# Performance work log

Hardware: AMD Instinct MI355X
Metric: run time of the kernel (lower is better)

## Reference

```python
import jax, jax.numpy as jnp
import numpy as np

MUL = 32            # multiplicity of 0e and 1o irreps
IN_DIM = MUL * 4    # 32 scalars + 32 vectors = 128
SH_DIM = 4          # 1x0e + 1x1o
N_EDGE_FEAT = 128
HIDDEN = 128
W_NUMEL = 4 * MUL * MUL  # 4 CG paths, uvw weights 32x1x32 each
EPS = 1e-5
INV_SQRT3 = 1.0 / np.sqrt(3.0)
PATH_NORM = 1.0 / np.sqrt(2.0 * MUL)  # 2 paths per output irrep, fan-in MUL


def _fc(edge_attr, W1, b1, W2, b2):
    h = jax.nn.relu(edge_attr @ W1 + b1)
    return h @ W2 + b2  # [E, W_NUMEL]


def _tensor_product(x, sh, w):
    # FullyConnectedTensorProduct for (32x0e+32x1o) x (1x0e+1x1o) -> (32x0e+32x1o)
    # CG (real w3j): 0x0->0: 1 ; 0x1->1, 1x0->1, 1x1->0: delta/sqrt(3)
    E = x.shape[0]
    x0 = x[:, :MUL]                      # [E,32]   scalars
    x1 = x[:, MUL:].reshape(E, MUL, 3)   # [E,32,3] vectors
    sh0 = sh[:, 0]                       # [E]
    sh1 = sh[:, 1:4]                     # [E,3]
    wA = w[:, 0 * MUL * MUL:1 * MUL * MUL].reshape(E, MUL, MUL)  # 0e x 0e -> 0e
    wB = w[:, 1 * MUL * MUL:2 * MUL * MUL].reshape(E, MUL, MUL)  # 0e x 1o -> 1o
    wC = w[:, 2 * MUL * MUL:3 * MUL * MUL].reshape(E, MUL, MUL)  # 1o x 0e -> 1o
    wD = w[:, 3 * MUL * MUL:4 * MUL * MUL].reshape(E, MUL, MUL)  # 1o x 1o -> 0e
    out0 = PATH_NORM * (
        jnp.einsum('eu,euw->ew', x0 * sh0[:, None], wA)
        + INV_SQRT3 * jnp.einsum('eui,ei,euw->ew', x1, sh1, wD))
    out1 = PATH_NORM * INV_SQRT3 * (
        jnp.einsum('eu,ei,euw->ewi', x0, sh1, wB)
        + jnp.einsum('eui,euw->ewi', x1 * sh0[:, None, None], wC))
    return jnp.concatenate([out0, out1.reshape(E, MUL * 3)], axis=-1)  # [E,128]


def _batch_norm(x, bn_weight, bn_bias):
    # e3nn-style equivariant BatchNorm (training stats): scalars get mean/var
    # normalization + affine; vectors get norm normalization + scale.
    N = x.shape[0]
    s = x[:, :MUL]                       # [N,32]
    v = x[:, MUL:].reshape(N, MUL, 3)    # [N,32,3]
    s = s - s.mean(axis=0)
    s = s * (jax.lax.rsqrt((s ** 2).mean(axis=0) + EPS) * bn_weight[:MUL]) + bn_bias
    v_norm = jax.lax.rsqrt((v ** 2).mean(axis=-1).mean(axis=0) + EPS)  # [32]
    v = v * (v_norm * bn_weight[MUL:])[None, :, None]
    return jnp.concatenate([s, v.reshape(N, MUL * 3)], axis=-1)


def _forward(node_attr, edge_index, edge_attr, edge_sh,
             W1, b1, W2, b2, bn_weight, bn_bias):
    edge_src, edge_dst = edge_index[0], edge_index[1]
    N = node_attr.shape[0]
    w = _fc(edge_attr, W1, b1, W2, b2)                     # [E, 4096]
    tp = _tensor_product(node_attr[edge_dst], edge_sh, w)  # [E, 128]
    # scatter mean over edge_src
    summed = jax.ops.segment_sum(tp, edge_src, num_segments=N)
    counts = jax.ops.segment_sum(jnp.ones((tp.shape[0],), tp.dtype), edge_src,
                                 num_segments=N)
    out = summed / jnp.maximum(counts, 1.0)[:, None]
    out = out + node_attr                                  # residual (same dim, pad=0)
    return _batch_norm(out, bn_weight, bn_bias)


def setup_inputs() -> dict:
    key = jax.random.key(0)
    ks = jax.random.split(key, 10)
    N, E = 10000, 60000
    node_attr = jax.random.normal(ks[0], (N, IN_DIM), jnp.float32)
    edge_index = jax.random.randint(ks[1], (2, E), 0, N)
    edge_attr = jax.random.normal(ks[2], (E, N_EDGE_FEAT), jnp.float32)
    edge_sh = jax.random.normal(ks[3], (E, SH_DIM), jnp.float32)
    W1 = jax.random.normal(ks[4], (N_EDGE_FEAT, HIDDEN), jnp.float32) / np.sqrt(N_EDGE_FEAT)
    b1 = jnp.zeros((HIDDEN,), jnp.float32)
    W2 = jax.random.normal(ks[5], (HIDDEN, W_NUMEL), jnp.float32) / np.sqrt(HIDDEN)
    b2 = jnp.zeros((W_NUMEL,), jnp.float32)
    bn_weight = jnp.ones((2 * MUL,), jnp.float32)
    bn_bias = jnp.zeros((MUL,), jnp.float32)
    return {"node_attr": node_attr, "edge_index": edge_index,
            "edge_attr": edge_attr, "edge_sh": edge_sh,
            "W1": W1, "b1": b1, "W2": W2, "b2": b2,
            "bn_weight": bn_weight, "bn_bias": bn_bias}


def reference(node_attr, edge_index, edge_attr, edge_sh,
              W1, b1, W2, b2, bn_weight, bn_bias):
    return _forward(node_attr, edge_index, edge_attr, edge_sh,
                    W1, b1, W2, b2, bn_weight, bn_bias)
```

## Files before the change

### kernel.cpp

```cpp
#include <hip/hip_runtime.h>
#include <math.h>

#define EPSV 1e-5f
#define IS3  0.57735026918962576f
#define PNRM 0.125f

typedef __attribute__((ext_vector_type(8)))  short  short8;
typedef __attribute__((ext_vector_type(16))) float  floatx16;

static __device__ inline unsigned short f2bf(float f) {
    unsigned int u = __float_as_uint(f);
    return (unsigned short)((u + 0x7fff + ((u >> 16) & 1)) >> 16);
}
static __device__ inline float bflo(unsigned int u) { return __uint_as_float(u << 16); }
static __device__ inline float bfhi(unsigned int u) { return __uint_as_float(u & 0xffff0000u); }

#define GLD16(gp, lp) __builtin_amdgcn_global_load_lds( \
    (const __attribute__((address_space(1))) unsigned int*)(gp), \
    (__attribute__((address_space(3))) unsigned int*)(lp), 16, 0, 0)

__global__ __launch_bounds__(256) void k0_sw(const float* __restrict__ src,
                                             unsigned short* __restrict__ dst,
                                             int total, int nc) {
    int i = blockIdx.x * 256 + threadIdx.x;
    if (i >= total) return;
    int tile = i >> 12, t = i & 4095;
    int k = ((t >> 8) << 3) | (t & 7);
    int c = (tile << 5) | ((t >> 3) & 31);
    dst[i] = f2bf(src[(size_t)k * nc + c]);
}

__global__ __launch_bounds__(256) void k1_fc(const float* __restrict__ ea,
                                             const unsigned short* __restrict__ W1T,
                                             const float* __restrict__ b1,
                                             const int* __restrict__ ei,
                                             unsigned short* __restrict__ h,
                                             int* __restrict__ deg, int E) {
    __shared__ __align__(16) unsigned short W1s[16384];
    __shared__ __align__(16) unsigned short outT[5120];
    const int tid = threadIdx.x, lane = tid & 63, wv = tid >> 6;
    const int half = lane >> 5, col = lane & 31;
    const int e0 = blockIdx.x * 128;

    if (tid < 128) { int e = e0 + tid; if (e < E) atomicAdd(&deg[ei[e]], 1); }

#pragma unroll
    for (int q = 0; q < 8; ++q) {
        int chunk = wv * 8 + q;
        GLD16((const char*)W1T + chunk * 1024 + lane * 16, (char*)W1s + chunk * 1024);
    }

    int e = e0 + wv * 32 + col; if (e >= E) e = E - 1;
    short8 afr[8];
#pragma unroll
    for (int c = 0; c < 8; ++c) {
        const float4* p = (const float4*)(ea + (size_t)e * 128 + c * 16 + half * 8);
        float4 f0 = p[0], f1 = p[1];
        short8 v;
        v[0] = (short)f2bf(f0.x); v[1] = (short)f2bf(f0.y);
        v[2] = (short)f2bf(f0.z); v[3] = (short)f2bf(f0.w);
        v[4] = (short)f2bf(f1.x); v[5] = (short)f2bf(f1.y);
        v[6] = (short)f2bf(f1.z); v[7] = (short)f2bf(f1.w);
        afr[c] = v;
    }
    __syncthreads();

#pragma unroll
    for (int jt = 0; jt < 4; ++jt) {
        floatx16 d = {0,0,0,0,0,0,0,0,0,0,0,0,0,0,0,0};
#pragma unroll
        for (int c = 0; c < 8; ++c) {
            short8 bf = *(const short8*)((const char*)W1s + jt * 8192 + (2 * c + half) * 512 + col * 16);
            d = __builtin_amdgcn_mfma_f32_32x32x16_bf16(afr[c], bf, d, 0, 0, 0);
        }
        float b1v = b1[jt * 32 + col];
#pragma unroll
        for (int reg = 0; reg < 16; ++reg) {
            int r = (reg & 3) + 8 * (reg >> 2) + 4 * half;
            float v = d[reg] + b1v;
            v = v > 0.f ? v : 0.f;
            outT[(wv * 32 + r) * 40 + col] = f2bf(v);
        }
        __syncthreads();
#pragma unroll
        for (int ps = 0; ps < 2; ++ps) {
            int lin = ps * 256 + tid;
            int row = lin >> 2, c8 = (lin & 3) * 8;
            int er = e0 + row;
            if (er < E) {
                short8 v = *(const short8*)&outT[row * 40 + c8];
                *(short8*)(h + (size_t)er * 128 + jt * 32 + c8) = v;
            }
        }
        __syncthreads();
    }
}

__global__ __launch_bounds__(256, 2) void k2_mfma(const unsigned short* __restrict__ h,
                                                  const unsigned short* __restrict__ W2T,
                                                  const float* __restrict__ b2,
                                                  const float* __restrict__ na,
                                                  const int* __restrict__ ei,
                                                  const float* __restrict__ sh,
                                                  float* __restrict__ tp, int E) {
    __shared__ __align__(16) char smem[42240];
    unsigned short* As  = (unsigned short*)smem;
    unsigned short* Ctb = (unsigned short*)(smem + 16384);
    float* shs = (float*)(smem + 40960);
    float* red = (float*)smem;

    const int tid = threadIdx.x, lane = tid & 63, wv = tid >> 6;
    const int half = lane >> 5, col = lane & 31;
    const int ust = wv >> 1, esub = wv & 1;
    const int e0 = blockIdx.x * 64;

    if (tid < 64) {
        int e = e0 + tid; int ec = e < E ? e : E - 1;
        float4 s = *(const float4*)(sh + (size_t)ec * 4);
        *(float4*)&shs[tid * 4] = s;
    }

    for (int idx = tid; idx < 2048; idx += 256) {
        int el = idx & 63, u = idx >> 6;
        int e = e0 + el; int ec = e < E ? e : E - 1;
        int dn = ei[E + ec];
        const float* nar = na + (size_t)dn * 128;
        float x0  = nar[u];
        float x10 = nar[32 + u * 3], x11 = nar[33 + u * 3], x12 = nar[34 + u * 3];
        const float* shr = sh + (size_t)ec * 4;
        float s0 = shr[0], s1 = shr[1], s2 = shr[2], s3 = shr[3];
        int o = u * 64 + el;
        Ctb[0 * 2048 + o] = f2bf(x0 * s0);
        Ctb[1 * 2048 + o] = f2bf(x0);
        Ctb[2 * 2048 + o] = f2bf(x10);
        Ctb[3 * 2048 + o] = f2bf(x11);
        Ctb[4 * 2048 + o] = f2bf(x12);
        Ctb[5 * 2048 + o] = f2bf(IS3 * (x10 * s1 + x11 * s2 + x12 * s3));
    }

#pragma unroll
    for (int q = 0; q < 4; ++q) {
        int t = wv * 4 + q;
        int g = t >> 3;
        int jj = (t & 7) * 64 + lane;
        int e = e0 + g * 32 + (jj & 31); int ec = e < E ? e : E - 1;
        GLD16((const char*)h + (size_t)ec * 256 + (jj >> 5) * 16,
              (char*)As + g * 8192 + (t & 7) * 1024);
    }
    __syncthreads();

    short8 afr[8];
#pragma unroll
    for (int c = 0; c < 8; ++c)
        afr[c] = *(const short8*)((const char*)As + esub * 8192 + (2 * c + half) * 512 + col * 16);

    float acc0[16] = {}, accB[16] = {}, accC0[16] = {}, accC1[16] = {}, accC2[16] = {};
    const int elb0 = esub * 32 + half * 4;
    const unsigned short* bbase = W2T + half * 256 + col * 8;

#define LOADB(p, br, b2r) do {                                         \
        int _ct = 2 * (p) + ust;                                       \
        const unsigned short* _bp = bbase + (size_t)_ct * 4096;        \
        _Pragma("unroll")                                              \
        for (int _c = 0; _c < 8; ++_c)                                 \
            (br)[_c] = *(const short8*)(_bp + _c * 512);               \
        (b2r) = b2[_ct * 32 + col];                                    \
    } while (0)

#define COMPUTE(p, br, b2v) do {                                                              \
        const int _ct = 2 * (p) + ust;                                                        \
        const int _b = _ct >> 5, _u = _ct & 31;                                               \
        floatx16 d = {0,0,0,0,0,0,0,0,0,0,0,0,0,0,0,0};                                       \
        _Pragma("unroll")                                                                     \
        for (int _c = 0; _c < 8; ++_c)                                                        \
            d = __builtin_amdgcn_mfma_f32_32x32x16_bf16(afr[_c], (br)[_c], d, 0, 0, 0);       \
        if (_b == 0 || _b == 3) {                                                             \
            const unsigned short* tb = Ctb + (_b == 0 ? 0 : 5) * 2048;                        \
            _Pragma("unroll")                                                                 \
            for (int q = 0; q < 4; ++q) {                                                     \
                uint2 cv = *(const uint2*)&tb[_u * 64 + elb0 + q * 8];                        \
                acc0[q * 4 + 0] += bflo(cv.x) * (d[q * 4 + 0] + (b2v));                       \
                acc0[q * 4 + 1] += bfhi(cv.x) * (d[q * 4 + 1] + (b2v));                       \
                acc0[q * 4 + 2] += bflo(cv.y) * (d[q * 4 + 2] + (b2v));                       \
                acc0[q * 4 + 3] += bfhi(cv.y) * (d[q * 4 + 3] + (b2v));                       \
            }                                                                                 \
        } else if (_b == 1) {                                                                 \
            _Pragma("unroll")                                                                 \
            for (int q = 0; q < 4; ++q) {                                                     \
                uint2 cv = *(const uint2*)&Ctb[1 * 2048 + _u * 64 + elb0 + q * 8];            \
                accB[q * 4 + 0] += bflo(cv.x) * (d[q * 4 + 0] + (b2v));                       \
                accB[q * 4 + 1] += bfhi(cv.x) * (d[q * 4 + 1] + (b2v));                       \
                accB[q * 4 + 2] += bflo(cv.y) * (d[q * 4 + 2] + (b2v));                       \
                accB[q * 4 + 3] += bfhi(cv.y) * (d[q * 4 + 3] + (b2v));                       \
            }                                                                                 \
        } else {                                                                              \
            _Pragma("unroll")                                                                 \
            for (int q = 0; q < 4; ++q) {                                                     \
                uint2 cu0 = *(const uint2*)&Ctb[2 * 2048 + _u * 64 + elb0 + q * 8];           \
                uint2 cu1 = *(const uint2*)&Ctb[3 * 2048 + _u * 64 + elb0 + q * 8];           \
                uint2 cu2 = *(const uint2*)&Ctb[4 * 2048 + _u * 64 + elb0 + q * 8];           \
                float f0[4] = {bflo(cu0.x), bfhi(cu0.x), bflo(cu0.y), bfhi(cu0.y)};           \
                float f1[4] = {bflo(cu1.x), bfhi(cu1.x), bflo(cu1.y), bfhi(cu1.y)};           \
                float f2[4] = {bflo(cu2.x), bfhi(cu2.x), bflo(cu2.y), bfhi(cu2.y)};           \
                _Pragma("unroll")                                                             \
                for (int rr = 0; rr < 4; ++rr) {                                              \
                    float v = d[q * 4 + rr] + (b2v);                                          \
                    accC0[q * 4 + rr] += f0[rr] * v;                                          \
                    accC1[q * 4 + rr] += f1[rr] * v;                                          \
                    accC2[q * 4 + rr] += f2[rr] * v;                                          \
                }                                                                             \
            }                                                                                 \
        }                                                                                     \
    } while (0)

    short8 bA[8], bB[8];
    float b2A, b2B;
    LOADB(0, bA, b2A);
    for (int p = 0; p < 64; p += 2) {
        LOADB(p + 1, bB, b2B);
        COMPUTE(p, bA, b2A);
        if (p + 2 < 64) LOADB(p + 2, bA, b2A);
        COMPUTE(p + 1, bB, b2B);
    }

    __syncthreads();
    if (ust == 1) {
#pragma unroll
        for (int reg = 0; reg < 16; ++reg) {
            red[(((esub * 5 + 0) * 16 + reg) << 6) + lane] = acc0[reg];
            red[(((esub * 5 + 1) * 16 + reg) << 6) + lane] = accB[reg];
            red[(((esub * 5 + 2) * 16 + reg) << 6) + lane] = accC0[reg];
            red[(((esub * 5 + 3) * 16 + reg) << 6) + lane] = accC1[reg];
            red[(((esub * 5 + 4) * 16 + reg) << 6) + lane] = accC2[reg];
        }
    }
    __syncthreads();
    if (ust == 0) {
#pragma unroll
        for (int q = 0; q < 4; ++q) {
#pragma unroll
            for (int rr = 0; rr < 4; ++rr) {
                int reg = q * 4 + rr;
                int el = esub * 32 + q * 8 + half * 4 + rr;
                int e = e0 + el;
                if (e >= E) continue;
                float a0  = acc0[reg]  + red[(((esub * 5 + 0) * 16 + reg) << 6) + lane];
                float aB  = accB[reg]  + red[(((esub * 5 + 1) * 16 + reg) << 6) + lane];
                float c0v = accC0[reg] + red[(((esub * 5 + 2) * 16 + reg) << 6) + lane];
                float c1v = accC1[reg] + red[(((esub * 5 + 3) * 16 + reg) << 6) + lane];
                float c2v = accC2[reg] + red[(((esub * 5 + 4) * 16 + reg) << 6) + lane];
                float4 sv = *(const float4*)&shs[el * 4];
                float* tpe = tp + (size_t)e * 128;
                tpe[col] = PNRM * a0;
                tpe[32 + col * 3 + 0] = PNRM * IS3 * (sv.y * aB + sv.x * c0v);
                tpe[32 + col * 3 + 1] = PNRM * IS3 * (sv.z * aB + sv.x * c1v);
                tpe[32 + col * 3 + 2] = PNRM * IS3 * (sv.w * aB + sv.x * c2v);
            }
        }
    }
#undef LOADB
#undef COMPUTE
}

__global__ __launch_bounds__(1024) void k_scan(const int* __restrict__ deg,
                                               int* __restrict__ rowptr, int N) {
    __shared__ int part[1024];
    const int tid = threadIdx.x;
    const int chunk = (N + 1023) / 1024;
    const int base = tid * chunk;
    int s = 0;
    for (int i = 0; i < chunk; ++i) {
        int n = base + i;
        if (n < N) s += deg[n];
    }
    part[tid] = s;
    __syncthreads();
    for (int off = 1; off < 1024; off <<= 1) {
        int t = 0;
        if (tid >= off) t = part[tid - off];
        __syncthreads();
        if (tid >= off) part[tid] += t;
        __syncthreads();
    }
    int prefix = (tid == 0) ? 0 : part[tid - 1];
    for (int i = 0; i < chunk; ++i) {
        int n = base + i;
        if (n < N) { rowptr[n] = prefix; prefix += deg[n]; }
    }
    if (tid == 0) rowptr[N] = part[1023];
}

__global__ __launch_bounds__(256) void k_fill(const int* __restrict__ ei,
                                              const int* __restrict__ rowptr,
                                              int* __restrict__ cursor,
                                              int* __restrict__ elist, int E) {
    int e = blockIdx.x * 256 + threadIdx.x;
    if (e >= E) return;
    int s = ei[e];
    int pos = rowptr[s] + atomicAdd(&cursor[s], 1);
    elist[pos] = e;
}

__global__ __launch_bounds__(256) void k4_gather(const float* __restrict__ tp,
                                                 const int* __restrict__ rowptr,
                                                 const int* __restrict__ elist,
                                                 const float* __restrict__ na,
                                                 float* __restrict__ pre,
                                                 float* __restrict__ stats, int N) {
    __shared__ float bns[96];
    const int tid = threadIdx.x;
    if (tid < 96) bns[tid] = 0.f;
    __syncthreads();
    const int o = tid & 127, hf = tid >> 7;
    for (int n = blockIdx.x * 2 + hf; n < N; n += gridDim.x * 2) {
        int r0 = rowptr[n], r1 = rowptr[n + 1];
        float s = 0.f;
        for (int j = r0; j < r1; ++j)
            s += tp[(size_t)elist[j] * 128 + o];
        int dg = r1 - r0;
        float cf = (float)(dg > 0 ? dg : 1);
        float v = s / cf + na[(size_t)n * 128 + o];
        pre[(size_t)n * 128 + o] = v;
        if (o < 32) {
            atomicAdd(&bns[o], v);
            atomicAdd(&bns[32 + o], v * v);
        } else {
            atomicAdd(&bns[64 + (o - 32) / 3], v * v);
        }
    }
    __syncthreads();
    if (tid < 96) atomicAdd(&stats[tid], bns[tid]);
}

__global__ __launch_bounds__(256) void k5_bn(const float* __restrict__ pre,
                                             const float* __restrict__ stats,
                                             const float* __restrict__ bnw,
                                             const float* __restrict__ bnb,
                                             float* __restrict__ out, int N) {
    size_t idx = (size_t)blockIdx.x * 256 + threadIdx.x;
    if (idx >= (size_t)N * 128) return;
    int o = (int)(idx & 127);
    float v = pre[idx];
    float invN = 1.f / (float)N;
    if (o < 32) {
        float m   = stats[o] * invN;
        float var = stats[32 + o] * invN - m * m;
        out[idx] = (v - m) * rsqrtf(var + EPSV) * bnw[o] + bnb[o];
    } else {
        int j = (o - 32) / 3;
        float vn = rsqrtf(stats[64 + j] * invN * (1.f / 3.f) + EPSV);
        out[idx] = v * vn * bnw[32 + j];
    }
}

extern "C" void kernel_launch(void* const* d_in, const int* in_sizes, int n_in,
                              void* d_out, int out_size, void* d_ws, size_t ws_size,
                              hipStream_t stream) {
    const float* node_attr  = (const float*)d_in[0];
    const int*   edge_index = (const int*)d_in[1];
    const float* edge_attr  = (const float*)d_in[2];
    const float* edge_sh    = (const float*)d_in[3];
    const float* W1  = (const float*)d_in[4];
    const float* b1  = (const float*)d_in[5];
    const float* W2  = (const float*)d_in[6];
    const float* b2  = (const float*)d_in[7];
    const float* bnw = (const float*)d_in[8];
    const float* bnb = (const float*)d_in[9];

    const int N = in_sizes[0] / 128;
    const int E = in_sizes[1] / 2;

    float* tp     = (float*)d_ws;
    float* pre    = tp + (size_t)E * 128;
    float* stats  = pre + (size_t)N * 128;
    int*   deg    = (int*)(stats + 96);
    int*   cursor = deg + N;
    int*   rowptr = cursor + N;
    int*   elist  = rowptr + N + 1;
    char* pbase = (char*)(elist + E);
    pbase += (16 - ((size_t)pbase & 15)) & 15;
    unsigned short* h   = (unsigned short*)pbase;
    unsigned short* W2T = h + (size_t)E * 128;
    unsigned short* W1T = W2T + (size_t)524288;

    hipMemsetAsync(stats, 0, (96 + 2 * (size_t)N) * sizeof(int), stream);

    k0_sw<<<(128 * 4096 + 255) / 256, 256, 0, stream>>>(W2, W2T, 128 * 4096, 4096);
    k0_sw<<<(128 * 128 + 255) / 256, 256, 0, stream>>>(W1, W1T, 128 * 128, 128);
    k1_fc<<<(E + 127) / 128, 256, 0, stream>>>(edge_attr, W1T, b1, edge_index, h, deg, E);
    k_scan<<<1, 1024, 0, stream>>>(deg, rowptr, N);
    k_fill<<<(E + 255) / 256, 256, 0, stream>>>(edge_index, rowptr, cursor, elist, E);
    k2_mfma<<<(E + 63) / 64, 256, 0, stream>>>(h, W2T, b2, node_attr, edge_index,
                                               edge_sh, tp, E);
    k4_gather<<<256, 256, 0, stream>>>(tp, rowptr, elist, node_attr, pre, stats, N);
    size_t ntot = (size_t)N * 128;
    k5_bn<<<(int)((ntot + 255) / 256), 256, 0, stream>>>(pre, stats, bnw, bnb,
                                                         (float*)d_out, N);
}
```

Before: 302.9 us.

## Fuse prep kernels, pre-swizzle hidden activations, fold TP scales, deepen B prefetch

Merges the two weight-transpose kernels and the memset into one tiled transpose kernel that also zeroes the workspace. It also folds the edge-list fill into k2 and has k1 write hidden activations in an MFMA-fragment-ready swizzled layout, so k2 loads A fragments directly and needs no LDS staging. Path-norm, 1/sqrt(3) and sh0 scales are folded into the bf16 C operand, which shrinks the cross-wave reduction from five accumulator sets to four. The B-operand prefetch goes from double to triple buffering, and the gather grid grows. Together these cut launches, barriers and LDS use, at the cost of more register pressure and bf16 rounding of the pre-scaled operands.

```diff
diff --git a/kernel.cpp b/kernel.cpp
--- a/kernel.cpp
+++ b/kernel.cpp
@@ -19,25 +19,51 @@
     (const __attribute__((address_space(1))) unsigned int*)(gp), \
     (__attribute__((address_space(3))) unsigned int*)(lp), 16, 0, 0)
 
-__global__ __launch_bounds__(256) void k0_sw(const float* __restrict__ src,
-                                             unsigned short* __restrict__ dst,
-                                             int total, int nc) {
-    int i = blockIdx.x * 256 + threadIdx.x;
-    if (i >= total) return;
-    int tile = i >> 12, t = i & 4095;
-    int k = ((t >> 8) << 3) | (t & 7);
-    int c = (tile << 5) | ((t >> 3) & 31);
-    dst[i] = f2bf(src[(size_t)k * nc + c]);
+__global__ __launch_bounds__(256) void k0_tile(const float* __restrict__ W2,
+                                               const float* __restrict__ W1,
+                                               unsigned short* __restrict__ W2T,
+                                               unsigned short* __restrict__ W1T,
+                                               int* __restrict__ zbase, int zn) {
+    const int bx = blockIdx.x, tid = threadIdx.x;
+    if (bx >= 132) {
+        int i = (bx - 132) * 256 + tid;
+        if (i < zn) zbase[i] = 0;
+        return;
+    }
+    __shared__ float tile[128 * 33];
+    const float* src;
+    unsigned short* dst;
+    int nc, tb;
+    if (bx < 128) { src = W2; dst = W2T; nc = 4096; tb = bx; }
+    else          { src = W1; dst = W1T; nc = 128;  tb = bx - 128; }
+    const int c0 = tb * 32;
+#pragma unroll
+    for (int r = 0; r < 16; ++r) {
+        int lin = r * 256 + tid;
+        int k = lin >> 5, c = lin & 31;
+        tile[k * 33 + c] = src[(size_t)k * nc + c0 + c];
+    }
+    __syncthreads();
+#pragma unroll
+    for (int r = 0; r < 2; ++r) {
+        int g = r * 256 + tid;
+        int kc = g >> 5, c = g & 31;
+        short8 v;
+#pragma unroll
+        for (int j = 0; j < 8; ++j)
+            v[j] = (short)f2bf(tile[(kc * 8 + j) * 33 + c]);
+        *(short8*)(dst + (size_t)tb * 4096 + kc * 256 + c * 8) = v;
+    }
 }
 
 __global__ __launch_bounds__(256) void k1_fc(const float* __restrict__ ea,
                                              const unsigned short* __restrict__ W1T,
                                              const float* __restrict__ b1,
                                              const int* __restrict__ ei,
-                                             unsigned short* __restrict__ h,
+                                             unsigned short* __restrict__ hsw,
                                              int* __restrict__ deg, int E) {
     __shared__ __align__(16) unsigned short W1s[16384];
-    __shared__ __align__(16) unsigned short outT[5120];
+    __shared__ __align__(16) unsigned short bounce[4 * 1056];
     const int tid = threadIdx.x, lane = tid & 63, wv = tid >> 6;
     const int half = lane >> 5, col = lane & 31;
     const int e0 = blockIdx.x * 128;
@@ -65,6 +91,8 @@
     }
     __syncthreads();
 
+    unsigned short* myb = bounce + wv * 1056;
+    const int gg = blockIdx.x * 4 + wv;
 #pragma unroll
     for (int jt = 0; jt < 4; ++jt) {
         floatx16 d = {0,0,0,0,0,0,0,0,0,0,0,0,0,0,0,0};
@@ -79,34 +107,28 @@
             int r = (reg & 3) + 8 * (reg >> 2) + 4 * half;
             float v = d[reg] + b1v;
             v = v > 0.f ? v : 0.f;
-            outT[(wv * 32 + r) * 40 + col] = f2bf(v);
-        }
-        __syncthreads();
-#pragma unroll
-        for (int ps = 0; ps < 2; ++ps) {
-            int lin = ps * 256 + tid;
-            int row = lin >> 2, c8 = (lin & 3) * 8;
-            int er = e0 + row;
-            if (er < E) {
-                short8 v = *(const short8*)&outT[row * 40 + c8];
-                *(short8*)(h + (size_t)er * 128 + jt * 32 + c8) = v;
-            }
-        }
-        __syncthreads();
-    }
-}
-
-__global__ __launch_bounds__(256, 2) void k2_mfma(const unsigned short* __restrict__ h,
+            myb[(col >> 3) * 264 + r * 8 + (col & 7)] = f2bf(v);
+        }
+#pragma unroll
+        for (int s = 0; s < 2; ++s) {
+            short8 v = *(const short8*)&myb[(s * 2 + (lane >> 5)) * 264 + (lane & 31) * 8];
+            *(short8*)(hsw + (size_t)gg * 4096 + jt * 1024 + s * 512 + lane * 8) = v;
+        }
+    }
+}
+
+__global__ __launch_bounds__(256, 2) void k2_mfma(const unsigned short* __restrict__ hsw,
                                                   const unsigned short* __restrict__ W2T,
                                                   const float* __restrict__ b2,
                                                   const float* __restrict__ na,
                                                   const int* __restrict__ ei,
                                                   const float* __restrict__ sh,
+                                                  const int* __restrict__ rowptr,
+                                                  int* __restrict__ cursor,
+                                                  int* __restrict__ elist,
                                                   float* __restrict__ tp, int E) {
-    __shared__ __align__(16) char smem[42240];
-    unsigned short* As  = (unsigned short*)smem;
-    unsigned short* Ctb = (unsigned short*)(smem + 16384);
-    float* shs = (float*)(smem + 40960);
+    __shared__ __align__(16) char smem[32768];
+    unsigned short* Ctb = (unsigned short*)smem;
     float* red = (float*)smem;
 
     const int tid = threadIdx.x, lane = tid & 63, wv = tid >> 6;
@@ -115,9 +137,12 @@
     const int e0 = blockIdx.x * 64;
 
     if (tid < 64) {
-        int e = e0 + tid; int ec = e < E ? e : E - 1;
-        float4 s = *(const float4*)(sh + (size_t)ec * 4);
-        *(float4*)&shs[tid * 4] = s;
+        int e = e0 + tid;
+        if (e < E) {
+            int s = ei[e];
+            int pos = rowptr[s] + atomicAdd(&cursor[s], 1);
+            elist[pos] = e;
+        }
     }
 
     for (int idx = tid; idx < 2048; idx += 256) {
@@ -130,29 +155,21 @@
         const float* shr = sh + (size_t)ec * 4;
         float s0 = shr[0], s1 = shr[1], s2 = shr[2], s3 = shr[3];
         int o = u * 64 + el;
-        Ctb[0 * 2048 + o] = f2bf(x0 * s0);
-        Ctb[1 * 2048 + o] = f2bf(x0);
-        Ctb[2 * 2048 + o] = f2bf(x10);
-        Ctb[3 * 2048 + o] = f2bf(x11);
-        Ctb[4 * 2048 + o] = f2bf(x12);
-        Ctb[5 * 2048 + o] = f2bf(IS3 * (x10 * s1 + x11 * s2 + x12 * s3));
-    }
-
-#pragma unroll
-    for (int q = 0; q < 4; ++q) {
-        int t = wv * 4 + q;
-        int g = t >> 3;
-        int jj = (t & 7) * 64 + lane;
-        int e = e0 + g * 32 + (jj & 31); int ec = e < E ? e : E - 1;
-        GLD16((const char*)h + (size_t)ec * 256 + (jj >> 5) * 16,
-              (char*)As + g * 8192 + (t & 7) * 1024);
-    }
-    __syncthreads();
-
+        Ctb[0 * 2048 + o] = f2bf(PNRM * x0 * s0);
+        Ctb[1 * 2048 + o] = f2bf(PNRM * IS3 * x0);
+        Ctb[2 * 2048 + o] = f2bf(PNRM * IS3 * s0 * x10);
+        Ctb[3 * 2048 + o] = f2bf(PNRM * IS3 * s0 * x11);
+        Ctb[4 * 2048 + o] = f2bf(PNRM * IS3 * s0 * x12);
+        Ctb[5 * 2048 + o] = f2bf(PNRM * IS3 * (x10 * s1 + x11 * s2 + x12 * s3));
+    }
+
+    const int gg = blockIdx.x * 2 + esub;
     short8 afr[8];
 #pragma unroll
     for (int c = 0; c < 8; ++c)
-        afr[c] = *(const short8*)((const char*)As + esub * 8192 + (2 * c + half) * 512 + col * 16);
+        afr[c] = *(const short8*)(hsw + (size_t)gg * 4096 + (2 * c + half) * 256 + col * 8);
+
+    __syncthreads();
 
     float acc0[16] = {}, accB[16] = {}, accC0[16] = {}, accC1[16] = {}, accC2[16] = {};
     const int elb0 = esub * 32 + half * 4;
@@ -213,25 +230,36 @@
         }                                                                                     \
     } while (0)
 
-    short8 bA[8], bB[8];
-    float b2A, b2B;
-    LOADB(0, bA, b2A);
-    for (int p = 0; p < 64; p += 2) {
-        LOADB(p + 1, bB, b2B);
-        COMPUTE(p, bA, b2A);
-        if (p + 2 < 64) LOADB(p + 2, bA, b2A);
-        COMPUTE(p + 1, bB, b2B);
-    }
+    short8 bA[8], bB[8], bC[8];
+    float b2A, b2B, b2C;
+    LOADB(0, bA, b2A); LOADB(1, bB, b2B); LOADB(2, bC, b2C);
+    for (int p = 0; p < 60; p += 3) {
+        COMPUTE(p,     bA, b2A); LOADB(p + 3, bA, b2A);
+        COMPUTE(p + 1, bB, b2B); LOADB(p + 4, bB, b2B);
+        COMPUTE(p + 2, bC, b2C); LOADB(p + 5, bC, b2C);
+    }
+    COMPUTE(60, bA, b2A); LOADB(63, bA, b2A);
+    COMPUTE(61, bB, b2B);
+    COMPUTE(62, bC, b2C);
+    COMPUTE(63, bA, b2A);
+#undef LOADB
+#undef COMPUTE
 
     __syncthreads();
     if (ust == 1) {
 #pragma unroll
-        for (int reg = 0; reg < 16; ++reg) {
-            red[(((esub * 5 + 0) * 16 + reg) << 6) + lane] = acc0[reg];
-            red[(((esub * 5 + 1) * 16 + reg) << 6) + lane] = accB[reg];
-            red[(((esub * 5 + 2) * 16 + reg) << 6) + lane] = accC0[reg];
-            red[(((esub * 5 + 3) * 16 + reg) << 6) + lane] = accC1[reg];
-            red[(((esub * 5 + 4) * 16 + reg) << 6) + lane] = accC2[reg];
+        for (int q = 0; q < 4; ++q) {
+#pragma unroll
+            for (int rr = 0; rr < 4; ++rr) {
+                int reg = q * 4 + rr;
+                int el = esub * 32 + q * 8 + half * 4 + rr;
+                int e = e0 + el; int ec = e < E ? e : E - 1;
+                float4 sv = *(const float4*)(sh + (size_t)ec * 4);
+                red[(((esub * 4 + 0) * 16 + reg) << 6) + lane] = acc0[reg];
+                red[(((esub * 4 + 1) * 16 + reg) << 6) + lane] = sv.y * accB[reg] + accC0[reg];
+                red[(((esub * 4 + 2) * 16 + reg) << 6) + lane] = sv.z * accB[reg] + accC1[reg];
+                red[(((esub * 4 + 3) * 16 + reg) << 6) + lane] = sv.w * accB[reg] + accC2[reg];
+            }
         }
     }
     __syncthreads();
@@ -244,22 +272,19 @@
                 int el = esub * 32 + q * 8 + half * 4 + rr;
                 int e = e0 + el;
                 if (e >= E) continue;
-                float a0  = acc0[reg]  + red[(((esub * 5 + 0) * 16 + reg) << 6) + lane];
-                float aB  = accB[reg]  + red[(((esub * 5 + 1) * 16 + reg) << 6) + lane];
-                float c0v = accC0[reg] + red[(((esub * 5 + 2) * 16 + reg) << 6) + lane];
-                float c1v = accC1[reg] + red[(((esub * 5 + 3) * 16 + reg) << 6) + lane];
-                float c2v = accC2[reg] + red[(((esub * 5 + 4) * 16 + reg) << 6) + lane];
-                float4 sv = *(const float4*)&shs[el * 4];
+                float4 sv = *(const float4*)(sh + (size_t)e * 4);
+                float a0 = acc0[reg] + red[(((esub * 4 + 0) * 16 + reg) << 6) + lane];
+                float o0 = sv.y * accB[reg] + accC0[reg] + red[(((esub * 4 + 1) * 16 + reg) << 6) + lane];
+                float o1 = sv.z * accB[reg] + accC1[reg] + red[(((esub * 4 + 2) * 16 + reg) << 6) + lane];
+                float o2 = sv.w * accB[reg] + accC2[reg] + red[(((esub * 4 + 3) * 16 + reg) << 6) + lane];
                 float* tpe = tp + (size_t)e * 128;
-                tpe[col] = PNRM * a0;
-                tpe[32 + col * 3 + 0] = PNRM * IS3 * (sv.y * aB + sv.x * c0v);
-                tpe[32 + col * 3 + 1] = PNRM * IS3 * (sv.z * aB + sv.x * c1v);
-                tpe[32 + col * 3 + 2] = PNRM * IS3 * (sv.w * aB + sv.x * c2v);
+                tpe[col] = a0;
+                tpe[32 + col * 3 + 0] = o0;
+                tpe[32 + col * 3 + 1] = o1;
+                tpe[32 + col * 3 + 2] = o2;
             }
         }
     }
-#undef LOADB
-#undef COMPUTE
 }
 
 __global__ __launch_bounds__(1024) void k_scan(const int* __restrict__ deg,
@@ -288,17 +313,6 @@
         if (n < N) { rowptr[n] = prefix; prefix += deg[n]; }
     }
     if (tid == 0) rowptr[N] = part[1023];
-}
-
-__global__ __launch_bounds__(256) void k_fill(const int* __restrict__ ei,
-                                              const int* __restrict__ rowptr,
-                                              int* __restrict__ cursor,
-                                              int* __restrict__ elist, int E) {
-    int e = blockIdx.x * 256 + threadIdx.x;
-    if (e >= E) return;
-    int s = ei[e];
-    int pos = rowptr[s] + atomicAdd(&cursor[s], 1);
-    elist[pos] = e;
 }
 
 __global__ __launch_bounds__(256) void k4_gather(const float* __restrict__ tp,
@@ -369,6 +383,7 @@
 
     const int N = in_sizes[0] / 128;
     const int E = in_sizes[1] / 2;
+    const int ngroups = ((E + 127) / 128) * 4;
 
     float* tp     = (float*)d_ws;
     float* pre    = tp + (size_t)E * 128;
@@ -379,20 +394,19 @@
     int*   elist  = rowptr + N + 1;
     char* pbase = (char*)(elist + E);
     pbase += (16 - ((size_t)pbase & 15)) & 15;
-    unsigned short* h   = (unsigned short*)pbase;
-    unsigned short* W2T = h + (size_t)E * 128;
+    unsigned short* hsw = (unsigned short*)pbase;
+    unsigned short* W2T = hsw + (size_t)ngroups * 4096;
     unsigned short* W1T = W2T + (size_t)524288;
 
-    hipMemsetAsync(stats, 0, (96 + 2 * (size_t)N) * sizeof(int), stream);
-
-    k0_sw<<<(128 * 4096 + 255) / 256, 256, 0, stream>>>(W2, W2T, 128 * 4096, 4096);
-    k0_sw<<<(128 * 128 + 255) / 256, 256, 0, stream>>>(W1, W1T, 128 * 128, 128);
-    k1_fc<<<(E + 127) / 128, 256, 0, stream>>>(edge_attr, W1T, b1, edge_index, h, deg, E);
+    const int zn = 96 + 2 * N;
+    const int zblocks = (zn + 255) / 256;
+
+    k0_tile<<<132 + zblocks, 256, 0, stream>>>(W2, W1, W2T, W1T, (int*)stats, zn);
+    k1_fc<<<(E + 127) / 128, 256, 0, stream>>>(edge_attr, W1T, b1, edge_index, hsw, deg, E);
     k_scan<<<1, 1024, 0, stream>>>(deg, rowptr, N);
-    k_fill<<<(E + 255) / 256, 256, 0, stream>>>(edge_index, rowptr, cursor, elist, E);
-    k2_mfma<<<(E + 63) / 64, 256, 0, stream>>>(h, W2T, b2, node_attr, edge_index,
-                                               edge_sh, tp, E);
-    k4_gather<<<256, 256, 0, stream>>>(tp, rowptr, elist, node_attr, pre, stats, N);
+    k2_mfma<<<(E + 63) / 64, 256, 0, stream>>>(hsw, W2T, b2, node_attr, edge_index,
+                                               edge_sh, rowptr, cursor, elist, tp, E);
+    k4_gather<<<1024, 256, 0, stream>>>(tp, rowptr, elist, node_attr, pre, stats, N);
     size_t ntot = (size_t)N * 128;
     k5_bn<<<(int)((ntot + 255) / 256), 256, 0, stream>>>(pre, stats, bnw, bnb,
                                                          (float*)d_out, N);
```

After: 260.0 us. 14.2% less time.
